# Optimization experiments

Hardware: AMD Instinct MI355X
Metric: run time of the kernel (lower is better)

The kernel has to match this reference:

```python
import jax, jax.numpy as jnp
import numpy as np


def setup_inputs() -> dict:
    key = jax.random.key(0)
    k1, k2, k3, k4 = jax.random.split(key, 4)
    B, idf, cdf, h, w, L = 32, 256, 256, 64, 64, 128
    x = jax.random.normal(k1, (B, idf, h, w), dtype=jnp.float32)
    context = jax.random.normal(k2, (B, cdf, L), dtype=jnp.float32)
    # conv1x1 weight (no bias): [idf, cdf]
    W = jax.random.normal(k3, (idf, cdf), dtype=jnp.float32) / np.sqrt(cdf)
    mask = jax.random.randint(k4, (B, L), 0, 2).astype(bool)
    return {"x": x, "context": context, "W": W, "mask": mask}


def reference(x, context, W, mask):
    B, idf, h, w = x.shape
    hxw = h * w
    L = context.shape[2]
    # conv1x1 projection of context: [B, idf, L]
    source = jnp.einsum('ic,bcl->bil', W, context)
    target = x.reshape(B, idf, hxw)
    # QK^T: [B, hxw, L]
    attn = jnp.einsum('bip,bil->bpl', target, source)
    # faithful to torch: mask [B, L] is tiled hxw times over the flattened
    # [B*hxw, L] view (row order b*hxw+p vs tile order p*B+b, as in original)
    attn_flat = attn.reshape(B * hxw, L)
    attn_flat = jnp.where(jnp.tile(mask, (hxw, 1)), -jnp.inf, attn_flat)
    attn = jax.nn.softmax(attn_flat, axis=-1).reshape(B, hxw, L)
    attn_t = jnp.swapaxes(attn, 1, 2)  # [B, L, hxw]
    # PV: [B, idf, hxw] -> [B, idf, h, w]
    result = jnp.einsum('bil,blp->bip', source, attn_t).reshape(B, idf, h, w)
    return result, attn_t.reshape(B, L, h, w)
```

## Files before the change

kernel.cpp:

```cpp
#include <hip/hip_runtime.h>
#include <cstdint>

#define IDF 256
#define CDF 256
#define NL  128
#define HXW 4096
#define NB  32
#define PTILE 64

typedef _Float16 f16x8 __attribute__((ext_vector_type(8)));
typedef float f32x4 __attribute__((ext_vector_type(4)));
typedef unsigned short u16;
typedef unsigned int u32;

union Frag { f16x8 v; u32 u[4]; uint2 u2[2]; };

__device__ __forceinline__ u16 f2h(float f) { union { _Float16 h; u16 s; } c; c.h = (_Float16)f; return c.s; }
__device__ __forceinline__ float h2f(u16 s) { union { _Float16 h; u16 s; } c; c.s = s; return (float)c.h; }
__device__ __forceinline__ u32 pk2(float a, float b) { return (u32)f2h(a) | ((u32)f2h(b) << 16); }


__global__ void prep_kernel(const u32* __restrict__ m, u32* __restrict__ ws0) {
  __shared__ int bi_s, bf_s, mode_s;
  if (threadIdx.x == 0) { bi_s = 0; bf_s = 0; }
  __syncthreads();
  int bi = 0, bfl = 0;
  for (int k = 0; k < 4; ++k) {
    u32 v = m[threadIdx.x * 4 + k];
    if (v > 1u) bi = 1;
    float f = __uint_as_float(v);
    if (!(f == 0.0f || f == 1.0f)) bfl = 1;
  }
  if (bi) atomicOr(&bi_s, 1);
  if (bfl) atomicOr(&bf_s, 1);
  __syncthreads();
  if (threadIdx.x == 0) { mode_s = (bi_s == 0) ? 0 : ((bf_s == 0) ? 1 : 2); ws0[0] = (u32)mode_s; }
  __syncthreads();
  const int mode = mode_s;
  if (threadIdx.x < 128) {
    int row = threadIdx.x >> 2, q = threadIdx.x & 3;
    u32 bits = 0;
    for (int c = 0; c < 32; ++c) {
      int idx = row * NL + q * 32 + c;
      int mv;
      if (mode == 0)      mv = ((const int*)m)[idx] != 0;
      else if (mode == 1) mv = ((const float*)m)[idx] != 0.0f;
      else                mv = ((const unsigned char*)m)[idx] != 0;
      bits |= (u32)mv << c;
    }
    ws0[64 + row * 4 + q] = bits;
  }
}

__global__ __launch_bounds__(256) void proj_kernel(const float* __restrict__ W,
                                                   const float* __restrict__ ctx,
                                                   u16* __restrict__ srcF,
                                                   u16* __restrict__ srcT) {
  __shared__ float sWt[16][33];
  __shared__ float sC[16 * NL];
  const int tid = threadIdx.x;
  const int b = blockIdx.y;
  const int i0 = blockIdx.x * 32;
  const int tx = tid & 31;
  const int ty = tid >> 5;
  float acc[4][4] = {};
  const float* ctxb = ctx + (size_t)b * CDF * NL;
  for (int c0 = 0; c0 < CDF; c0 += 16) {
    if (tid < 128) {
      int i = tid >> 2, cq = tid & 3;
      float4 w4 = *(const float4*)(W + (size_t)(i0 + i) * CDF + c0 + cq * 4);
      sWt[cq * 4 + 0][i] = w4.x; sWt[cq * 4 + 1][i] = w4.y;
      sWt[cq * 4 + 2][i] = w4.z; sWt[cq * 4 + 3][i] = w4.w;
    }
#pragma unroll
    for (int k = 0; k < 2; ++k) {
      int idx = tid + k * 256;
      int r = idx >> 5, c4 = idx & 31;
      *(float4*)(sC + r * NL + c4 * 4) =
          *(const float4*)(ctxb + (size_t)(c0 + r) * NL + c4 * 4);
    }
    __syncthreads();
#pragma unroll
    for (int cc = 0; cc < 16; ++cc) {
      float4 c4 = *(const float4*)(sC + cc * NL + tx * 4);
#pragma unroll
      for (int ii = 0; ii < 4; ++ii) {
        float w = sWt[cc][ty * 4 + ii];
        acc[ii][0] = fmaf(w, c4.x, acc[ii][0]);
        acc[ii][1] = fmaf(w, c4.y, acc[ii][1]);
        acc[ii][2] = fmaf(w, c4.z, acc[ii][2]);
        acc[ii][3] = fmaf(w, c4.w, acc[ii][3]);
      }
    }
    __syncthreads();
  }
  u16* sf = srcF + (size_t)b * IDF * NL;
  u16* st = srcT + (size_t)b * NL * IDF;
#pragma unroll
  for (int ii = 0; ii < 4; ++ii) {
    int i = i0 + ty * 4 + ii;
    u32 d0 = pk2(acc[ii][0], acc[ii][1]);
    u32 d1 = pk2(acc[ii][2], acc[ii][3]);
    *(uint2*)(sf + (size_t)i * NL + tx * 4) = make_uint2(d0, d1);
#pragma unroll
    for (int jl = 0; jl < 4; ++jl)
      st[(size_t)(tx * 4 + jl) * IDF + i] = f2h(acc[ii][jl]);
  }
}

__global__ __launch_bounds__(256) void attn_kernel(
    const float* __restrict__ x, const u16* __restrict__ srcF,
    const u16* __restrict__ srcT, const u32* __restrict__ wsm,
    float* __restrict__ out0, float* __restrict__ out1) {
  __shared__ __align__(16) u16 sA[64 * 132];
  __shared__ __align__(16) u16 sXT[64 * 44];
  __shared__ __align__(16) u16 sST[128 * 44];

  const int tid = threadIdx.x;
  const int lane = tid & 63;
  const int w = tid >> 6;
  const int m15 = lane & 15;
  const int g = lane >> 4;
  const int b = blockIdx.y;
  const int p0 = blockIdx.x * PTILE;

  f32x4 accq[8];
#pragma unroll
  for (int nt = 0; nt < 8; ++nt) accq[nt] = f32x4{0.f, 0.f, 0.f, 0.f};

  const float* xb = x + (size_t)b * IDF * HXW + p0;
  const u16* stb = srcT + (size_t)b * NL * IDF;
  const int kp = tid >> 4;
  const int p4 = (tid & 15) * 4;
  const int sl = tid >> 1;
  const int sh = tid & 1;

  u32* xd = (u32*)sXT;
  u32* sd = (u32*)sST;

  for (int ic = 0; ic < 8; ++ic) {
    const float* xp = xb + (size_t)(ic * 32 + kp * 2) * HXW + p4;
    float4 xa = *(const float4*)xp;
    float4 xc = *(const float4*)(xp + HXW);
    const u16* sp = stb + (size_t)sl * IDF + ic * 32 + sh * 16;
    uint4 s0 = *(const uint4*)sp;
    uint4 s1 = *(const uint4*)(sp + 8);
    xd[(p4 + 0) * 22 + kp] = pk2(xa.x, xc.x);
    xd[(p4 + 1) * 22 + kp] = pk2(xa.y, xc.y);
    xd[(p4 + 2) * 22 + kp] = pk2(xa.z, xc.z);
    xd[(p4 + 3) * 22 + kp] = pk2(xa.w, xc.w);
    int sb0 = sl * 22 + sh * 8;
    *(uint2*)(sd + sb0 + 0) = make_uint2(s0.x, s0.y);
    *(uint2*)(sd + sb0 + 2) = make_uint2(s0.z, s0.w);
    *(uint2*)(sd + sb0 + 4) = make_uint2(s1.x, s1.y);
    *(uint2*)(sd + sb0 + 6) = make_uint2(s1.z, s1.w);
    __syncthreads();
    Frag af;
    {
      const u32* xr = (const u32*)sXT + (w * 16 + m15) * 22 + g * 4;
      af.u2[0] = *(const uint2*)xr;
      af.u2[1] = *(const uint2*)(xr + 2);
    }
#pragma unroll
    for (int nt = 0; nt < 8; ++nt) {
      Frag bf;
      const u32* br = (const u32*)sST + (nt * 16 + m15) * 22 + g * 4;
      bf.u2[0] = *(const uint2*)br;
      bf.u2[1] = *(const uint2*)(br + 2);
      accq[nt] = __builtin_amdgcn_mfma_f32_16x16x32_f16(af.v, bf.v, accq[nt], 0, 0, 0);
    }
    __syncthreads();
  }

  const int prow = w * 16 + g * 4;
#pragma unroll
  for (int r = 0; r < 4; ++r) {
    int rm = (prow + r) & 31;
    uint4 mr = *(const uint4*)(wsm + rm * 4);
    u32 mw[4] = {mr.x, mr.y, mr.z, mr.w};
    float mx = -3.0e38f;
#pragma unroll
    for (int nt = 0; nt < 8; ++nt) {
      u32 bits = mw[nt >> 1] >> ((nt & 1) * 16);
      if ((bits >> m15) & 1u) accq[nt][r] = -3.0e38f;
      mx = fmaxf(mx, accq[nt][r]);
    }
    mx = fmaxf(mx, __shfl_xor(mx, 1));
    mx = fmaxf(mx, __shfl_xor(mx, 2));
    mx = fmaxf(mx, __shfl_xor(mx, 4));
    mx = fmaxf(mx, __shfl_xor(mx, 8));
    float e[8];
    float s = 0.f;
#pragma unroll
    for (int nt = 0; nt < 8; ++nt) { e[nt] = __expf(accq[nt][r] - mx); s += e[nt]; }
    s += __shfl_xor(s, 1); s += __shfl_xor(s, 2);
    s += __shfl_xor(s, 4); s += __shfl_xor(s, 8);
    float inv = 1.0f / s;
#pragma unroll
    for (int nt = 0; nt < 8; ++nt)
      sA[(prow + r) * 132 + nt * 16 + m15] = f2h(e[nt] * inv);
  }
  __syncthreads();

  float* o1 = out1 + (size_t)b * NL * HXW + p0;
  const int po = (tid & 7) * 8;
  const int lb = tid >> 3;
#pragma unroll
  for (int pass = 0; pass < 4; ++pass) {
    int l = pass * 32 + lb;
    float4 v0, v1;
    v0.x = h2f(sA[(po + 0) * 132 + l]); v0.y = h2f(sA[(po + 1) * 132 + l]);
    v0.z = h2f(sA[(po + 2) * 132 + l]); v0.w = h2f(sA[(po + 3) * 132 + l]);
    v1.x = h2f(sA[(po + 4) * 132 + l]); v1.y = h2f(sA[(po + 5) * 132 + l]);
    v1.z = h2f(sA[(po + 6) * 132 + l]); v1.w = h2f(sA[(po + 7) * 132 + l]);
    *(float4*)(o1 + (size_t)l * HXW + po) = v0;
    *(float4*)(o1 + (size_t)l * HXW + po + 4) = v1;
  }

  f32x4 accp[4][4];
#pragma unroll
  for (int mt = 0; mt < 4; ++mt)
#pragma unroll
    for (int nt2 = 0; nt2 < 4; ++nt2) accp[mt][nt2] = f32x4{0.f, 0.f, 0.f, 0.f};

  const u16* sfb = srcF + (size_t)b * IDF * NL;
  const u32* sAd = (const u32*)sA;
#pragma unroll
  for (int ks = 0; ks < 4; ++ks) {
    Frag af[4], bf[4];
#pragma unroll
    for (int mt = 0; mt < 4; ++mt) {
      int row = w * 64 + mt * 16 + m15;
      uint4 t = *(const uint4*)(sfb + (size_t)row * NL + ks * 32 + g * 8);
      af[mt].u[0] = t.x; af[mt].u[1] = t.y; af[mt].u[2] = t.z; af[mt].u[3] = t.w;
    }
#pragma unroll
    for (int nt2 = 0; nt2 < 4; ++nt2) {
      int di = (nt2 * 16 + m15) * 66 + ks * 16 + g * 4;
      bf[nt2].u2[0] = *(const uint2*)(sAd + di);
      bf[nt2].u2[1] = *(const uint2*)(sAd + di + 2);
    }
#pragma unroll
    for (int mt = 0; mt < 4; ++mt)
#pragma unroll
      for (int nt2 = 0; nt2 < 4; ++nt2)
        accp[mt][nt2] = __builtin_amdgcn_mfma_f32_16x16x32_f16(af[mt].v, bf[nt2].v, accp[mt][nt2], 0, 0, 0);
  }

  float* o0 = out0 + (size_t)b * IDF * HXW + p0;
#pragma unroll
  for (int mt = 0; mt < 4; ++mt)
#pragma unroll
    for (int nt2 = 0; nt2 < 4; ++nt2) {
      int col = nt2 * 16 + m15;
#pragma unroll
      for (int r = 0; r < 4; ++r) {
        int row = w * 64 + mt * 16 + g * 4 + r;
        o0[(size_t)row * HXW + col] = accp[mt][nt2][r];
      }
    }
}

extern "C" void kernel_launch(void* const* d_in, const int* in_sizes, int n_in,
                              void* d_out, int out_size, void* d_ws, size_t ws_size,
                              hipStream_t stream) {
  const float* x   = (const float*)d_in[0];
  const float* ctx = (const float*)d_in[1];
  const float* W   = (const float*)d_in[2];
  const void*  msk = d_in[3];
  float* out0 = (float*)d_out;
  float* out1 = out0 + (size_t)NB * IDF * HXW;
  u32* ws0 = (u32*)d_ws;
  u16* srcF = (u16*)((char*)d_ws + 1024);
  u16* srcT = (u16*)((char*)d_ws + 1024 + 2097152);

  prep_kernel<<<1, 256, 0, stream>>>((const u32*)msk, ws0);
  proj_kernel<<<dim3(8, NB), 256, 0, stream>>>(W, ctx, srcF, srcT);
  attn_kernel<<<dim3(HXW / PTILE, NB), 256, 0, stream>>>(x, srcF, srcT, ws0 + 64, out0, out1);
}
```

Measured before the change: 131.9 us.

## Transpose QK MFMA to load x directly into registers, drop LDS staging

```diff
diff --git a/kernel.cpp b/kernel.cpp
--- a/kernel.cpp
+++ b/kernel.cpp
@@ -9,15 +9,19 @@
 #define PTILE 64
 
 typedef _Float16 f16x8 __attribute__((ext_vector_type(8)));
+typedef __fp16 fp16x2 __attribute__((ext_vector_type(2)));
 typedef float f32x4 __attribute__((ext_vector_type(4)));
 typedef unsigned short u16;
 typedef unsigned int u32;
 
-union Frag { f16x8 v; u32 u[4]; uint2 u2[2]; };
+union Frag { f16x8 v; u32 u[4]; uint2 u2[2]; uint4 u4; };
 
 __device__ __forceinline__ u16 f2h(float f) { union { _Float16 h; u16 s; } c; c.h = (_Float16)f; return c.s; }
-__device__ __forceinline__ float h2f(u16 s) { union { _Float16 h; u16 s; } c; c.s = s; return (float)c.h; }
-__device__ __forceinline__ u32 pk2(float a, float b) { return (u32)f2h(a) | ((u32)f2h(b) << 16); }
+__device__ __forceinline__ u32 pkrtz(float a, float b) {
+  union { fp16x2 v; u32 u; } c;
+  c.v = __builtin_amdgcn_cvt_pkrtz(a, b);
+  return c.u;
+}
 
 
 __global__ void prep_kernel(const u32* __restrict__ m, u32* __restrict__ ws0) {
@@ -99,8 +103,8 @@
 #pragma unroll
   for (int ii = 0; ii < 4; ++ii) {
     int i = i0 + ty * 4 + ii;
-    u32 d0 = pk2(acc[ii][0], acc[ii][1]);
-    u32 d1 = pk2(acc[ii][2], acc[ii][3]);
+    u32 d0 = pkrtz(acc[ii][0], acc[ii][1]);
+    u32 d1 = pkrtz(acc[ii][2], acc[ii][3]);
     *(uint2*)(sf + (size_t)i * NL + tx * 4) = make_uint2(d0, d1);
 #pragma unroll
     for (int jl = 0; jl < 4; ++jl)
@@ -108,13 +112,11 @@
   }
 }
 
-__global__ __launch_bounds__(256) void attn_kernel(
+__global__ __launch_bounds__(256, 4) void attn_kernel(
     const float* __restrict__ x, const u16* __restrict__ srcF,
     const u16* __restrict__ srcT, const u32* __restrict__ wsm,
     float* __restrict__ out0, float* __restrict__ out1) {
   __shared__ __align__(16) u16 sA[64 * 132];
-  __shared__ __align__(16) u16 sXT[64 * 44];
-  __shared__ __align__(16) u16 sST[128 * 44];
 
   const int tid = threadIdx.x;
   const int lane = tid & 63;
@@ -123,99 +125,74 @@
   const int g = lane >> 4;
   const int b = blockIdx.y;
   const int p0 = blockIdx.x * PTILE;
+  const int pl = w * 16 + m15;
 
   f32x4 accq[8];
 #pragma unroll
   for (int nt = 0; nt < 8; ++nt) accq[nt] = f32x4{0.f, 0.f, 0.f, 0.f};
 
-  const float* xb = x + (size_t)b * IDF * HXW + p0;
   const u16* stb = srcT + (size_t)b * NL * IDF;
-  const int kp = tid >> 4;
-  const int p4 = (tid & 15) * 4;
-  const int sl = tid >> 1;
-  const int sh = tid & 1;
-
-  u32* xd = (u32*)sXT;
-  u32* sd = (u32*)sST;
-
+  const float* xcol = x + (size_t)b * IDF * HXW + p0 + pl;
+
+#pragma unroll 2
   for (int ic = 0; ic < 8; ++ic) {
-    const float* xp = xb + (size_t)(ic * 32 + kp * 2) * HXW + p4;
-    float4 xa = *(const float4*)xp;
-    float4 xc = *(const float4*)(xp + HXW);
-    const u16* sp = stb + (size_t)sl * IDF + ic * 32 + sh * 16;
-    uint4 s0 = *(const uint4*)sp;
-    uint4 s1 = *(const uint4*)(sp + 8);
-    xd[(p4 + 0) * 22 + kp] = pk2(xa.x, xc.x);
-    xd[(p4 + 1) * 22 + kp] = pk2(xa.y, xc.y);
-    xd[(p4 + 2) * 22 + kp] = pk2(xa.z, xc.z);
-    xd[(p4 + 3) * 22 + kp] = pk2(xa.w, xc.w);
-    int sb0 = sl * 22 + sh * 8;
-    *(uint2*)(sd + sb0 + 0) = make_uint2(s0.x, s0.y);
-    *(uint2*)(sd + sb0 + 2) = make_uint2(s0.z, s0.w);
-    *(uint2*)(sd + sb0 + 4) = make_uint2(s1.x, s1.y);
-    *(uint2*)(sd + sb0 + 6) = make_uint2(s1.z, s1.w);
-    __syncthreads();
-    Frag af;
-    {
-      const u32* xr = (const u32*)sXT + (w * 16 + m15) * 22 + g * 4;
-      af.u2[0] = *(const uint2*)xr;
-      af.u2[1] = *(const uint2*)(xr + 2);
-    }
+    float xv[8];
+#pragma unroll
+    for (int j = 0; j < 8; ++j)
+      xv[j] = xcol[(size_t)(ic * 32 + g * 8 + j) * HXW];
+    Frag bx;
+    bx.u[0] = pkrtz(xv[0], xv[1]); bx.u[1] = pkrtz(xv[2], xv[3]);
+    bx.u[2] = pkrtz(xv[4], xv[5]); bx.u[3] = pkrtz(xv[6], xv[7]);
 #pragma unroll
     for (int nt = 0; nt < 8; ++nt) {
-      Frag bf;
-      const u32* br = (const u32*)sST + (nt * 16 + m15) * 22 + g * 4;
-      bf.u2[0] = *(const uint2*)br;
-      bf.u2[1] = *(const uint2*)(br + 2);
-      accq[nt] = __builtin_amdgcn_mfma_f32_16x16x32_f16(af.v, bf.v, accq[nt], 0, 0, 0);
-    }
-    __syncthreads();
-  }
-
-  const int prow = w * 16 + g * 4;
-#pragma unroll
-  for (int r = 0; r < 4; ++r) {
-    int rm = (prow + r) & 31;
-    uint4 mr = *(const uint4*)(wsm + rm * 4);
-    u32 mw[4] = {mr.x, mr.y, mr.z, mr.w};
-    float mx = -3.0e38f;
-#pragma unroll
-    for (int nt = 0; nt < 8; ++nt) {
-      u32 bits = mw[nt >> 1] >> ((nt & 1) * 16);
-      if ((bits >> m15) & 1u) accq[nt][r] = -3.0e38f;
+      Frag af;
+      af.u4 = *(const uint4*)(stb + (size_t)(nt * 16 + m15) * IDF + ic * 32 + g * 8);
+      accq[nt] = __builtin_amdgcn_mfma_f32_16x16x32_f16(af.v, bx.v, accq[nt], 0, 0, 0);
+    }
+  }
+
+  const int rm = pl & 31;
+  uint4 mr = *(const uint4*)(wsm + rm * 4);
+  u32 mw[4] = {mr.x, mr.y, mr.z, mr.w};
+  float mx = -3.0e38f;
+#pragma unroll
+  for (int nt = 0; nt < 8; ++nt) {
+    u32 bits = mw[nt >> 1] >> ((nt & 1) * 16);
+#pragma unroll
+    for (int r = 0; r < 4; ++r) {
+      if ((bits >> (g * 4 + r)) & 1u) accq[nt][r] = -3.0e38f;
       mx = fmaxf(mx, accq[nt][r]);
     }
-    mx = fmaxf(mx, __shfl_xor(mx, 1));
-    mx = fmaxf(mx, __shfl_xor(mx, 2));
-    mx = fmaxf(mx, __shfl_xor(mx, 4));
-    mx = fmaxf(mx, __shfl_xor(mx, 8));
-    float e[8];
-    float s = 0.f;
-#pragma unroll
-    for (int nt = 0; nt < 8; ++nt) { e[nt] = __expf(accq[nt][r] - mx); s += e[nt]; }
-    s += __shfl_xor(s, 1); s += __shfl_xor(s, 2);
-    s += __shfl_xor(s, 4); s += __shfl_xor(s, 8);
-    float inv = 1.0f / s;
-#pragma unroll
-    for (int nt = 0; nt < 8; ++nt)
-      sA[(prow + r) * 132 + nt * 16 + m15] = f2h(e[nt] * inv);
-  }
-  __syncthreads();
-
-  float* o1 = out1 + (size_t)b * NL * HXW + p0;
-  const int po = (tid & 7) * 8;
-  const int lb = tid >> 3;
-#pragma unroll
-  for (int pass = 0; pass < 4; ++pass) {
-    int l = pass * 32 + lb;
-    float4 v0, v1;
-    v0.x = h2f(sA[(po + 0) * 132 + l]); v0.y = h2f(sA[(po + 1) * 132 + l]);
-    v0.z = h2f(sA[(po + 2) * 132 + l]); v0.w = h2f(sA[(po + 3) * 132 + l]);
-    v1.x = h2f(sA[(po + 4) * 132 + l]); v1.y = h2f(sA[(po + 5) * 132 + l]);
-    v1.z = h2f(sA[(po + 6) * 132 + l]); v1.w = h2f(sA[(po + 7) * 132 + l]);
-    *(float4*)(o1 + (size_t)l * HXW + po) = v0;
-    *(float4*)(o1 + (size_t)l * HXW + po + 4) = v1;
-  }
+  }
+  mx = fmaxf(mx, __shfl_xor(mx, 16));
+  mx = fmaxf(mx, __shfl_xor(mx, 32));
+  float s = 0.f;
+#pragma unroll
+  for (int nt = 0; nt < 8; ++nt)
+#pragma unroll
+    for (int r = 0; r < 4; ++r) {
+      float e = __expf(accq[nt][r] - mx);
+      accq[nt][r] = e;
+      s += e;
+    }
+  s += __shfl_xor(s, 16);
+  s += __shfl_xor(s, 32);
+  const float inv = 1.0f / s;
+
+  float* o1 = out1 + (size_t)b * NL * HXW + p0 + pl;
+  u32* sAd = (u32*)sA;
+#pragma unroll
+  for (int nt = 0; nt < 8; ++nt) {
+#pragma unroll
+    for (int r = 0; r < 4; ++r) {
+      float v = accq[nt][r] * inv;
+      accq[nt][r] = v;
+      o1[(size_t)(nt * 16 + g * 4 + r) * HXW] = v;
+    }
+    sAd[pl * 66 + nt * 8 + g * 2 + 0] = pkrtz(accq[nt][0], accq[nt][1]);
+    sAd[pl * 66 + nt * 8 + g * 2 + 1] = pkrtz(accq[nt][2], accq[nt][3]);
+  }
+  __syncthreads();
 
   f32x4 accp[4][4];
 #pragma unroll
@@ -224,16 +201,12 @@
     for (int nt2 = 0; nt2 < 4; ++nt2) accp[mt][nt2] = f32x4{0.f, 0.f, 0.f, 0.f};
 
   const u16* sfb = srcF + (size_t)b * IDF * NL;
-  const u32* sAd = (const u32*)sA;
 #pragma unroll
   for (int ks = 0; ks < 4; ++ks) {
     Frag af[4], bf[4];
 #pragma unroll
-    for (int mt = 0; mt < 4; ++mt) {
-      int row = w * 64 + mt * 16 + m15;
-      uint4 t = *(const uint4*)(sfb + (size_t)row * NL + ks * 32 + g * 8);
-      af[mt].u[0] = t.x; af[mt].u[1] = t.y; af[mt].u[2] = t.z; af[mt].u[3] = t.w;
-    }
+    for (int mt = 0; mt < 4; ++mt)
+      af[mt].u4 = *(const uint4*)(sfb + (size_t)(w * 64 + mt * 16 + m15) * NL + ks * 32 + g * 8);
 #pragma unroll
     for (int nt2 = 0; nt2 < 4; ++nt2) {
       int di = (nt2 * 16 + m15) * 66 + ks * 16 + g * 4;
```

After: 177.9 us. 1.35x slower.
